# Performance work log

Measured on AMD Instinct MI355X. Metric: run time of the kernel, lower is better.

## Reference

```python
import jax, jax.numpy as jnp
import numpy as np

HEAD_NUM = 16
EMBED = 1024

def setup_inputs() -> dict:
    key = jax.random.key(0)
    k1, k2, k3 = jax.random.split(key, 3)
    x = jax.random.normal(k1, (2, 2048, EMBED), dtype=jnp.float32)
    W_qkv = jax.random.normal(k2, (3 * EMBED, EMBED), dtype=jnp.float32) * (EMBED ** -0.5)
    W_out = jax.random.normal(k3, (EMBED, EMBED), dtype=jnp.float32) * (EMBED ** -0.5)
    return {"x": x, "W_qkv": W_qkv, "W_out": W_out}

def reference(x, W_qkv, W_out):
    b, t, E = x.shape
    h = HEAD_NUM
    d = E // h
    dk = (E / h) ** 0.5
    qkv = x @ W_qkv.T  # [b, t, 3E]
    # einops 'b t (d k h) -> k b h t d' with k=3, h=head_num (d outermost in the split)
    qkv = qkv.reshape(b, t, d, 3, h).transpose(3, 0, 4, 1, 2)  # [3, b, h, t, d]
    q, k, v = qkv[0], qkv[1], qkv[2]
    energy = jnp.einsum('bhid,bhjd->bhij', q, k) / dk  # [b, h, t, t]
    attn = jax.nn.softmax(energy, axis=-1)
    out = jnp.einsum('bhij,bhjd->bhid', attn, v)  # [b, h, t, d]
    out = out.transpose(0, 2, 1, 3).reshape(b, t, E)  # 'b h t d -> b t (h d)'
    return out @ W_out.T
```

## Files before the change

### kernel.cpp

```cpp
#include <hip/hip_runtime.h>
#include <hip/hip_bf16.h>


#define HEADS 16
#define EMB   1024
#define HDIM  64
#define BB    2
#define TT    2048
#define QSCALE 0.18033688011112042f

typedef __attribute__((ext_vector_type(8)))  short      bf16x8;
typedef __attribute__((ext_vector_type(8)))  _Float16   f16x8;
typedef __attribute__((ext_vector_type(4)))  float      f32x4;
typedef __attribute__((ext_vector_type(16))) float      f32x16;
typedef __attribute__((ext_vector_type(4)))  unsigned   u32x4;

__device__ __forceinline__ unsigned short f2bf(float f) {
    __hip_bfloat16 h = __float2bfloat16(f);
    return __builtin_bit_cast(unsigned short, h);
}
__device__ __forceinline__ float fexp2(float x) {
#if __has_builtin(__builtin_amdgcn_exp2f)
    return __builtin_amdgcn_exp2f(x);
#else
    return exp2f(x);
#endif
}
__device__ __forceinline__ unsigned pkrtz(float a, float b) {
    auto r = __builtin_amdgcn_cvt_pkrtz(a, b);
    return __builtin_bit_cast(unsigned, r);
}
__device__ __forceinline__ unsigned short f2h(float f) {
    return (unsigned short)(pkrtz(f, 0.f) & 0xffffu);
}
__device__ __forceinline__ float h2f(unsigned short u) {
    return (float)__builtin_bit_cast(_Float16, u);
}
__device__ __forceinline__ void gload_lds16(const void* g, void* l) {
    __builtin_amdgcn_global_load_lds(
        (const __attribute__((address_space(1))) void*)g,
        (__attribute__((address_space(3))) void*)l, 16, 0, 0);
}
__device__ __forceinline__ int swzi(int row, int blk) {
    return row * 64 + ((blk ^ (row & 7)) << 3);
}
__device__ __forceinline__ void pl32swap(unsigned& a, unsigned& b) {
    asm("v_permlane32_swap_b32 %0, %1" : "+v"(a), "+v"(b));
}

__global__ __launch_bounds__(256)
void conv_all(const float* __restrict__ x,    unsigned short* __restrict__ xb,
              const float* __restrict__ Wqkv, unsigned short* __restrict__ Wqb,
              const float* __restrict__ Wout, unsigned short* __restrict__ Wob) {
    const int blk = blockIdx.x;
    if (blk < 2048) {
        const int i = blk * 256 + threadIdx.x;
        const float4 v0 = ((const float4*)x)[i * 2];
        const float4 v1 = ((const float4*)x)[i * 2 + 1];
        ushort4 a, b;
        a.x = f2bf(v0.x); a.y = f2bf(v0.y); a.z = f2bf(v0.z); a.w = f2bf(v0.w);
        b.x = f2bf(v1.x); b.y = f2bf(v1.y); b.z = f2bf(v1.z); b.w = f2bf(v1.w);
        ((ushort4*)xb)[i * 2]     = a;
        ((ushort4*)xb)[i * 2 + 1] = b;
    } else if (blk < 5120) {
        const int np = blk - 2048;
        const int ns = (np & 63) * 48 + (np >> 10) * 16 + ((np >> 6) & 15);
        const float4 v = ((const float4*)(Wqkv + (size_t)ns * 1024))[threadIdx.x];
        ushort4 u;
        u.x = f2bf(v.x); u.y = f2bf(v.y); u.z = f2bf(v.z); u.w = f2bf(v.w);
        ((ushort4*)(Wqb + (size_t)np * 1024))[threadIdx.x] = u;
    } else {
        const int np = blk - 5120;
        const float4 v = ((const float4*)(Wout + (size_t)np * 1024))[threadIdx.x];
        ushort4 u;
        u.x = f2bf(v.x); u.y = f2bf(v.y); u.z = f2bf(v.z); u.w = f2bf(v.w);
        ((ushort4*)(Wob + (size_t)np * 1024))[threadIdx.x] = u;
    }
}

template<int EPI>
__global__ __launch_bounds__(256)
void gemm_bf16(const unsigned short* __restrict__ Ag,
               const unsigned short* __restrict__ Wg,
               float* __restrict__ Cout,
               unsigned short* __restrict__ QKb,
               unsigned short* __restrict__ Vt) {
    __shared__ __align__(16) unsigned short AbL[2][128 * 32];
    __shared__ __align__(16) unsigned short WbL[2][128 * 32];

    const int tid = threadIdx.x, lane = tid & 63, w = tid >> 6;
    const int n0 = blockIdx.x * 128, m0 = blockIdx.y * 128;
    const int wn = (w >> 1) * 64, wm = (w & 1) * 64;
    const int r16 = lane & 15, g = lane >> 4;
    const int goff = ((g ^ ((r16 >> 1) & 3)) << 3);

    f32x4 acc[4][4];
    #pragma unroll
    for (int i = 0; i < 4; ++i)
        #pragma unroll
        for (int j = 0; j < 4; ++j)
            acc[i][j] = (f32x4){0.f, 0.f, 0.f, 0.f};

    const int srow = w * 16 + (lane >> 2);
    const int scol = ((lane & 3) ^ ((lane >> 3) & 3)) << 3;
    const int sdst = (w * 16) * 32;
    const unsigned short* Asrc = Ag + (size_t)(m0 + srow) * 1024 + scol;
    const unsigned short* Wsrc = Wg + (size_t)(n0 + srow) * 1024 + scol;

#define STAGE(AB, WB, K0)                                            \
    do {                                                             \
        gload_lds16(Asrc + (K0),              (AB) + sdst);          \
        gload_lds16(Asrc + (K0) + 64 * 1024,  (AB) + sdst + 2048);   \
        gload_lds16(Wsrc + (K0),              (WB) + sdst);          \
        gload_lds16(Wsrc + (K0) + 64 * 1024,  (WB) + sdst + 2048);   \
    } while (0)

    unsigned short *pa0 = &AbL[0][0], *pa1 = &AbL[1][0];
    unsigned short *pw0 = &WbL[0][0], *pw1 = &WbL[1][0];

    STAGE(pa0, pw0, 0);

    for (int kt = 0; kt < 32; ++kt) {
        asm volatile("s_waitcnt vmcnt(0)" ::: "memory");
        __builtin_amdgcn_s_barrier();
        if (kt < 31) STAGE(pa1, pw1, (kt + 1) * 32);

        bf16x8 xf[4];
        #pragma unroll
        for (int mi = 0; mi < 4; ++mi)
            xf[mi] = *(const bf16x8*)&pa0[(wm + mi * 16 + r16) * 32 + goff];
        __builtin_amdgcn_s_setprio(1);
        #pragma unroll
        for (int ni = 0; ni < 4; ++ni) {
            const bf16x8 wf = *(const bf16x8*)&pw0[(wn + ni * 16 + r16) * 32 + goff];
            #pragma unroll
            for (int mi = 0; mi < 4; ++mi)
                acc[ni][mi] = __builtin_amdgcn_mfma_f32_16x16x32_bf16(
                    wf, xf[mi], acc[ni][mi], 0, 0, 0);
        }
        __builtin_amdgcn_s_setprio(0);

        unsigned short* t;
        t = pa0; pa0 = pa1; pa1 = t;
        t = pw0; pw0 = pw1; pw1 = t;
    }
#undef STAGE

    const int gq = g * 4;
    if (EPI == 0) {
        #pragma unroll
        for (int ni = 0; ni < 4; ++ni)
            #pragma unroll
            for (int mi = 0; mi < 4; ++mi) {
                const int m = m0 + wm + mi * 16 + r16;
                *(f32x4*)&Cout[(size_t)m * 1024 + (n0 + wn + ni * 16 + gq)] =
                    acc[ni][mi];
            }
    } else if (n0 < 2048) {
        #pragma unroll
        for (int ni = 0; ni < 4; ++ni) {
            const float qs = (n0 + wn + ni * 16) < 1024 ? QSCALE : 1.0f;
            #pragma unroll
            for (int mi = 0; mi < 4; ++mi) {
                const int m  = m0 + wm + mi * 16 + r16;
                const int np = n0 + wn + ni * 16 + gq;
                ushort4 u;
                u.x = f2bf(acc[ni][mi][0] * qs); u.y = f2bf(acc[ni][mi][1] * qs);
                u.z = f2bf(acc[ni][mi][2] * qs); u.w = f2bf(acc[ni][mi][3] * qs);
                *(ushort4*)&QKb[(size_t)m * 2048 + np] = u;
            }
        }
    } else {
        const int b = m0 >> 11, t0 = m0 & 2047;
        #pragma unroll
        for (int ni = 0; ni < 4; ++ni)
            #pragma unroll
            for (int mi = 0; mi < 4; ++mi) {
                const int t   = t0 + wm + mi * 16 + r16;
                const int nv0 = (n0 - 2048) + wn + ni * 16 + gq;
                #pragma unroll
                for (int j = 0; j < 4; ++j) {
                    const int nv = nv0 + j, h = nv >> 6, d = nv & 63;
                    Vt[(((size_t)(b * HEADS + h)) * HDIM + d) * TT + t] =
                        f2h(acc[ni][mi][j]);
                }
            }
    }
}

__global__ __launch_bounds__(256, 4)
void attn32(const unsigned short* __restrict__ QKb,
            const unsigned short* __restrict__ Vt,
            unsigned short* __restrict__ PO0,
            unsigned short* __restrict__ PO1,
            float* __restrict__ PL0,
            float* __restrict__ PL1) {
    __shared__ __align__(16) unsigned short Ks[2][64 * 64];
    __shared__ __align__(16) unsigned short Vs[2][64 * 64];

    const int tid = threadIdx.x, lane = tid & 63, w = tid >> 6;
    const int l31 = lane & 31, hi = lane >> 5;
    const int bid = blockIdx.x + 32 * blockIdx.y + 512 * blockIdx.z;
    const int vb  = (bid & 7) * 128 + (bid >> 3);
    const int qt  = vb & 15, kh = (vb >> 4) & 1;
    const int h   = (vb >> 5) & 15, b = vb >> 9;
    const int kbase = kh * 1024;
    const unsigned short* Vsrc = Vt + (size_t)(b * HEADS + h) * HDIM * TT;
    unsigned short* PO = kh ? PO1 : PO0;
    float*          PL = kh ? PL1 : PL0;

    bf16x8 qf[4];
    {
        const unsigned short* qrow =
            QKb + ((size_t)(b * TT + qt * 128 + w * 32 + l31)) * 2048 + h * HDIM;
        #pragma unroll
        for (int dc = 0; dc < 4; ++dc)
            qf[dc] = *(const bf16x8*)(qrow + dc * 16 + hi * 8);
    }

    const f32x16 zz = {};
    f32x16 o0 = {}, o1 = {};
    float lrun = 0.f;

    const int srl = lane >> 3;
    const int scb = lane & 7;
    const int cbs = (scb ^ srl) << 3;
    const int rl0 = w * 16 + srl;
    const unsigned short* kp0 =
        QKb + (size_t)(b * TT + kbase + rl0) * 2048 + 1024 + h * HDIM + cbs;
    const unsigned short* kp1 = kp0 + (size_t)8 * 2048;
    const unsigned short* vp0 = Vsrc + (size_t)rl0 * TT + kbase + cbs;
    const unsigned short* vp1 = vp0 + (size_t)8 * TT;
    unsigned short* const kd0 = &Ks[0][(w * 16) * 64];
    unsigned short* const kd1 = &Ks[1][(w * 16) * 64];
    unsigned short* const vd0 = &Vs[0][(w * 16) * 64];
    unsigned short* const vd1 = &Vs[1][(w * 16) * 64];

#define STAGE(KD, VD)                                                  \
    do {                                                               \
        gload_lds16(kp0, (KD));        gload_lds16(kp1, (KD) + 512);   \
        gload_lds16(vp0, (VD));        gload_lds16(vp1, (VD) + 512);   \
        kp0 += 64 * 2048; kp1 += 64 * 2048; vp0 += 64; vp1 += 64;      \
    } while (0)

    STAGE(kd0, vd0);

    for (int jt = 0; jt < 16; ++jt) {
        const int bb = jt & 1;
        __syncthreads();
        if (jt < 15) {
            if (bb) STAGE(kd0, vd0); else STAGE(kd1, vd1);
        }
        const unsigned short* KsB = &Ks[bb][0];
        const unsigned short* VsB = &Vs[bb][0];

        f32x16 stA, stB;
        __builtin_amdgcn_s_setprio(1);
        #pragma unroll
        for (int dc = 0; dc < 4; ++dc) {
            const bf16x8 kaA = *(const bf16x8*)&KsB[swzi(l31,      dc * 2 + hi)];
            const bf16x8 kaB = *(const bf16x8*)&KsB[swzi(32 + l31, dc * 2 + hi)];
            if (dc == 0) {
                stA = __builtin_amdgcn_mfma_f32_32x32x16_bf16(kaA, qf[0], zz, 0, 0, 0);
                stB = __builtin_amdgcn_mfma_f32_32x32x16_bf16(kaB, qf[0], zz, 0, 0, 0);
            } else {
                stA = __builtin_amdgcn_mfma_f32_32x32x16_bf16(kaA, qf[dc], stA, 0, 0, 0);
                stB = __builtin_amdgcn_mfma_f32_32x32x16_bf16(kaB, qf[dc], stB, 0, 0, 0);
            }
        }
        __builtin_amdgcn_s_setprio(0);

        #pragma unroll
        for (int x = 0; x < 2; ++x) {
            const f32x16& st = x ? stB : stA;
            float sum;
            unsigned wd[8];
            #pragma unroll
            for (int c = 0; c < 4; ++c) {
                const float e0 = fexp2(st[4 * c + 0]);
                const float e1 = fexp2(st[4 * c + 1]);
                const float e2 = fexp2(st[4 * c + 2]);
                const float e3 = fexp2(st[4 * c + 3]);
                const float s4 = (e0 + e1) + (e2 + e3);
                sum = c ? sum + s4 : s4;
                wd[2 * c]     = pkrtz(e0, e1);
                wd[2 * c + 1] = pkrtz(e2, e3);
            }
            lrun += sum;

            unsigned a0 = wd[0], a2 = wd[2];  pl32swap(a0, a2);
            unsigned a1 = wd[1], a3 = wd[3];  pl32swap(a1, a3);
            unsigned b0 = wd[4], b2 = wd[6];  pl32swap(b0, b2);
            unsigned b1 = wd[5], b3 = wd[7];  pl32swap(b1, b3);
            const u32x4 fva = {a0, a1, a2, a3};
            const u32x4 fvb = {b0, b1, b2, b3};
            const f16x8 pa0 = __builtin_bit_cast(f16x8, fva);
            const f16x8 pa1 = __builtin_bit_cast(f16x8, fvb);

            const int f0 = 2 * x;
            __builtin_amdgcn_s_setprio(1);
            {
                const f16x8 vb00 = *(const f16x8*)&VsB[swzi(l31,      f0 * 2 + hi)];
                const f16x8 vb01 = *(const f16x8*)&VsB[swzi(32 + l31, f0 * 2 + hi)];
                o0 = __builtin_amdgcn_mfma_f32_32x32x16_f16(pa0, vb00, o0, 0, 0, 0);
                o1 = __builtin_amdgcn_mfma_f32_32x32x16_f16(pa0, vb01, o1, 0, 0, 0);
                const f16x8 vb10 = *(const f16x8*)&VsB[swzi(l31,      (f0 + 1) * 2 + hi)];
                const f16x8 vb11 = *(const f16x8*)&VsB[swzi(32 + l31, (f0 + 1) * 2 + hi)];
                o0 = __builtin_amdgcn_mfma_f32_32x32x16_f16(pa1, vb10, o0, 0, 0, 0);
                o1 = __builtin_amdgcn_mfma_f32_32x32x16_f16(pa1, vb11, o1, 0, 0, 0);
            }
            __builtin_amdgcn_s_setprio(0);
        }
    }
#undef STAGE

    lrun += __shfl_xor(lrun, 32);
    const float inv = 1.0f / lrun;
    #pragma unroll
    for (int r = 0; r < 16; ++r) {
        const int qr = (r & 3) + 8 * (r >> 2) + 4 * hi;
        const float ir = __shfl(inv, qr);
        const int q = qt * 128 + w * 32 + qr;
        unsigned short* dst = PO + ((size_t)(b * TT + q)) * EMB + h * HDIM + l31;
        dst[0]  = f2h(o0[r] * ir);
        dst[32] = f2h(o1[r] * ir);
    }
    if (!hi) {
        const int q = qt * 128 + w * 32 + l31;
        PL[((size_t)(b * HEADS + h)) * TT + q] = lrun;
    }
}

__global__ __launch_bounds__(256)
void merge_attn(const unsigned short* __restrict__ PO0,
                const unsigned short* __restrict__ PO1,
                const float* __restrict__ PL0,
                const float* __restrict__ PL1,
                unsigned short* __restrict__ AOb) {
    const int i = blockIdx.x * 256 + threadIdx.x;
    const int tg  = i >> 8;
    const int col = (i & 255) * 4;
    const int h   = col >> 6;
    const int b   = tg >> 11, t = tg & 2047;

    const float la = PL0[((size_t)(b * HEADS + h)) * TT + t];
    const float lb = PL1[((size_t)(b * HEADS + h)) * TT + t];
    const float inv = 1.0f / (la + lb);
    const float wa = la * inv, wb = lb * inv;

    const ushort4 a = ((const ushort4*)PO0)[i];
    const ushort4 c = ((const ushort4*)PO1)[i];
    ushort4 o;
    o.x = f2bf(h2f(a.x) * wa + h2f(c.x) * wb);
    o.y = f2bf(h2f(a.y) * wa + h2f(c.y) * wb);
    o.z = f2bf(h2f(a.z) * wa + h2f(c.z) * wb);
    o.w = f2bf(h2f(a.w) * wa + h2f(c.w) * wb);
    ((ushort4*)AOb)[i] = o;
}

extern "C" void kernel_launch(void* const* d_in, const int* in_sizes, int n_in,
                              void* d_out, int out_size, void* d_ws, size_t ws_size,
                              hipStream_t stream) {
    const float* x    = (const float*)d_in[0];
    const float* Wqkv = (const float*)d_in[1];
    const float* Wout = (const float*)d_in[2];
    float* out = (float*)d_out;

    unsigned short* Wqb = (unsigned short*)d_ws;
    unsigned short* Wob = Wqb + 3145728;
    unsigned short* xb  = Wob + 1048576;
    unsigned short* QKb = xb  + 4194304;
    unsigned short* Vt  = QKb + 8388608;
    unsigned short* PO0 = Vt  + 4194304;
    unsigned short* PO1 = PO0 + 4194304;
    float*          PL0 = (float*)(PO1 + 4194304);
    float*          PL1 = PL0 + 65536;
    unsigned short* AOb = xb;

    conv_all<<<6144, 256, 0, stream>>>(x, xb, Wqkv, Wqb, Wout, Wob);

    gemm_bf16<1><<<dim3(24, 32), 256, 0, stream>>>(xb, Wqb, nullptr, QKb, Vt);

    attn32<<<dim3(32, 16, 2), 256, 0, stream>>>(QKb, Vt, PO0, PO1, PL0, PL1);

    merge_attn<<<4096, 256, 0, stream>>>(PO0, PO1, PL0, PL1, AOb);

    gemm_bf16<0><<<dim3(8, 32), 256, 0, stream>>>(AOb, Wob, out, nullptr, nullptr);
}
```

Baseline: 127.9 us.

## Use dedicated 256x192-tile, 512-thread GEMM kernel for QKV projection

Replaces the 128x128-tile templated GEMM for the QKV projection with a new 512-thread kernel that uses 256x192 output tiles and a K-step of 64 with swizzled LDS and double buffering. Each wave computes a 128x48 sub-tile, which raises operand reuse and arithmetic intensity and cuts global loads and barriers per FLOP. The grid becomes 256 blocks, exactly one per CU on a 256-CU part. This gives a single wave of work but less latency hiding, plus higher register and LDS pressure. The output GEMM is de-templated to its plain fp32 epilogue.

```diff
diff --git a/kernel.cpp b/kernel.cpp
--- a/kernel.cpp
+++ b/kernel.cpp
@@ -78,13 +78,112 @@
     }
 }
 
-template<int EPI>
+__global__ __launch_bounds__(512, 2)
+void gemm256_qkv(const unsigned short* __restrict__ Ag,
+                 const unsigned short* __restrict__ Wg,
+                 unsigned short* __restrict__ QKb,
+                 unsigned short* __restrict__ Vt) {
+    __shared__ __align__(16) unsigned short AbL[2][256 * 64];
+    __shared__ __align__(16) unsigned short BbL[2][192 * 64];
+
+    const int tid = threadIdx.x, lane = tid & 63, w = tid >> 6;
+    const int n0 = blockIdx.x * 192, m0 = blockIdx.y * 256;
+    const int wm = (w >> 2) * 128;
+    const int wn = (w & 3) * 48;
+    const int r16 = lane & 15, g = lane >> 4, gq = g * 4;
+
+    f32x4 acc[8][3];
+    #pragma unroll
+    for (int i = 0; i < 8; ++i)
+        #pragma unroll
+        for (int j = 0; j < 3; ++j)
+            acc[i][j] = (f32x4){0.f, 0.f, 0.f, 0.f};
+
+    const int srl = lane >> 3;
+    const int scol = ((lane & 7) ^ srl) << 3;
+    const unsigned short* Asrc = Ag + (size_t)(m0 + w * 32 + srl) * 1024 + scol;
+    const unsigned short* Bsrc = Wg + (size_t)(n0 + w * 24 + srl) * 1024 + scol;
+
+#define STAGE256(AB, BB, K0)                                                \
+    do {                                                                    \
+        _Pragma("unroll")                                                   \
+        for (int i = 0; i < 4; ++i)                                         \
+            gload_lds16(Asrc + (K0) + i * 8192,                             \
+                        (AB) + (w * 32 + i * 8) * 64);                      \
+        _Pragma("unroll")                                                   \
+        for (int i = 0; i < 3; ++i)                                         \
+            gload_lds16(Bsrc + (K0) + i * 8192,                             \
+                        (BB) + (w * 24 + i * 8) * 64);                      \
+    } while (0)
+
+    unsigned short *pa0 = &AbL[0][0], *pa1 = &AbL[1][0];
+    unsigned short *pb0 = &BbL[0][0], *pb1 = &BbL[1][0];
+
+    STAGE256(pa0, pb0, 0);
+
+    for (int kt = 0; kt < 16; ++kt) {
+        asm volatile("s_waitcnt vmcnt(0)" ::: "memory");
+        __builtin_amdgcn_s_barrier();
+        if (kt < 15) STAGE256(pa1, pb1, (kt + 1) * 64);
+
+        __builtin_amdgcn_s_setprio(1);
+        #pragma unroll
+        for (int ks = 0; ks < 2; ++ks) {
+            bf16x8 bf[3];
+            #pragma unroll
+            for (int ni = 0; ni < 3; ++ni)
+                bf[ni] = *(const bf16x8*)&pb0[swzi(wn + ni * 16 + r16, ks * 4 + g)];
+            #pragma unroll
+            for (int mi = 0; mi < 8; ++mi) {
+                const bf16x8 xf = *(const bf16x8*)&pa0[swzi(wm + mi * 16 + r16, ks * 4 + g)];
+                #pragma unroll
+                for (int ni = 0; ni < 3; ++ni)
+                    acc[mi][ni] = __builtin_amdgcn_mfma_f32_16x16x32_bf16(
+                        bf[ni], xf, acc[mi][ni], 0, 0, 0);
+            }
+        }
+        __builtin_amdgcn_s_setprio(0);
+
+        unsigned short* t;
+        t = pa0; pa0 = pa1; pa1 = t;
+        t = pb0; pb0 = pb1; pb1 = t;
+    }
+#undef STAGE256
+
+    #pragma unroll
+    for (int ni = 0; ni < 3; ++ni) {
+        const int npb = n0 + wn + ni * 16;
+        if (npb < 2048) {
+            const float qs = npb < 1024 ? QSCALE : 1.0f;
+            #pragma unroll
+            for (int mi = 0; mi < 8; ++mi) {
+                const int m = m0 + wm + mi * 16 + r16;
+                ushort4 u;
+                u.x = f2bf(acc[mi][ni][0] * qs); u.y = f2bf(acc[mi][ni][1] * qs);
+                u.z = f2bf(acc[mi][ni][2] * qs); u.w = f2bf(acc[mi][ni][3] * qs);
+                *(ushort4*)&QKb[(size_t)m * 2048 + npb + gq] = u;
+            }
+        } else {
+            #pragma unroll
+            for (int mi = 0; mi < 8; ++mi) {
+                const int m  = m0 + wm + mi * 16 + r16;
+                const int b  = m >> 11, tt = m & 2047;
+                const int nv0 = npb - 2048 + gq;
+                #pragma unroll
+                for (int j = 0; j < 4; ++j) {
+                    const int nv = nv0 + j, h = nv >> 6, d = nv & 63;
+                    Vt[(((size_t)(b * HEADS + h)) * HDIM + d) * TT + tt] =
+                        f2h(acc[mi][ni][j]);
+                }
+            }
+        }
+    }
+}
+
 __global__ __launch_bounds__(256)
 void gemm_bf16(const unsigned short* __restrict__ Ag,
                const unsigned short* __restrict__ Wg,
-               float* __restrict__ Cout,
-               unsigned short* __restrict__ QKb,
-               unsigned short* __restrict__ Vt) {
+               float* __restrict__ Cout) {
     __shared__ __align__(16) unsigned short AbL[2][128 * 32];
     __shared__ __align__(16) unsigned short WbL[2][128 * 32];
 
@@ -147,45 +246,14 @@
 #undef STAGE
 
     const int gq = g * 4;
-    if (EPI == 0) {
-        #pragma unroll
-        for (int ni = 0; ni < 4; ++ni)
-            #pragma unroll
-            for (int mi = 0; mi < 4; ++mi) {
-                const int m = m0 + wm + mi * 16 + r16;
-                *(f32x4*)&Cout[(size_t)m * 1024 + (n0 + wn + ni * 16 + gq)] =
-                    acc[ni][mi];
-            }
-    } else if (n0 < 2048) {
-        #pragma unroll
-        for (int ni = 0; ni < 4; ++ni) {
-            const float qs = (n0 + wn + ni * 16) < 1024 ? QSCALE : 1.0f;
-            #pragma unroll
-            for (int mi = 0; mi < 4; ++mi) {
-                const int m  = m0 + wm + mi * 16 + r16;
-                const int np = n0 + wn + ni * 16 + gq;
-                ushort4 u;
-                u.x = f2bf(acc[ni][mi][0] * qs); u.y = f2bf(acc[ni][mi][1] * qs);
-                u.z = f2bf(acc[ni][mi][2] * qs); u.w = f2bf(acc[ni][mi][3] * qs);
-                *(ushort4*)&QKb[(size_t)m * 2048 + np] = u;
-            }
-        }
-    } else {
-        const int b = m0 >> 11, t0 = m0 & 2047;
-        #pragma unroll
-        for (int ni = 0; ni < 4; ++ni)
-            #pragma unroll
-            for (int mi = 0; mi < 4; ++mi) {
-                const int t   = t0 + wm + mi * 16 + r16;
-                const int nv0 = (n0 - 2048) + wn + ni * 16 + gq;
-                #pragma unroll
-                for (int j = 0; j < 4; ++j) {
-                    const int nv = nv0 + j, h = nv >> 6, d = nv & 63;
-                    Vt[(((size_t)(b * HEADS + h)) * HDIM + d) * TT + t] =
-                        f2h(acc[ni][mi][j]);
-                }
-            }
-    }
+    #pragma unroll
+    for (int ni = 0; ni < 4; ++ni)
+        #pragma unroll
+        for (int mi = 0; mi < 4; ++mi) {
+            const int m = m0 + wm + mi * 16 + r16;
+            *(f32x4*)&Cout[(size_t)m * 1024 + (n0 + wn + ni * 16 + gq)] =
+                acc[ni][mi];
+        }
 }
 
 __global__ __launch_bounds__(256, 4)
@@ -379,11 +447,11 @@
 
     conv_all<<<6144, 256, 0, stream>>>(x, xb, Wqkv, Wqb, Wout, Wob);
 
-    gemm_bf16<1><<<dim3(24, 32), 256, 0, stream>>>(xb, Wqb, nullptr, QKb, Vt);
+    gemm256_qkv<<<dim3(16, 16), 512, 0, stream>>>(xb, Wqb, QKb, Vt);
 
     attn32<<<dim3(32, 16, 2), 256, 0, stream>>>(QKb, Vt, PO0, PO1, PL0, PL1);
 
     merge_attn<<<4096, 256, 0, stream>>>(PO0, PO1, PL0, PL1, AOb);
 
-    gemm_bf16<0><<<dim3(8, 32), 256, 0, stream>>>(AOb, Wob, out, nullptr, nullptr);
-}
+    gemm_bf16<<<dim3(8, 32), 256, 0, stream>>>(AOb, Wob, out);
+}
```

Measured after the change: 126.1 us (median of 2 runs). About the same (-1.4%).
